# Kernel optimization log

Measured on AMD Instinct MI355X. Metric: run time of the kernel, lower is better.

Reference implementation:

```python
import jax, jax.numpy as jnp
import numpy as np

B, N, D, H = 2, 4096, 512, 8
HD = D // H

def setup_inputs() -> dict:
    key = jax.random.key(0)
    ks = jax.random.split(key, 5)
    s = 1.0 / np.sqrt(D)
    return {
        "x": jax.random.normal(ks[0], (B, N, D), dtype=jnp.float32),
        "W_qkv": jax.random.uniform(ks[1], (D, 3 * D), minval=-s, maxval=s, dtype=jnp.float32),
        "b_qkv": jax.random.uniform(ks[2], (3 * D,), minval=-s, maxval=s, dtype=jnp.float32),
        "W_out": jax.random.uniform(ks[3], (D, D), minval=-s, maxval=s, dtype=jnp.float32),
        "b_out": jax.random.uniform(ks[4], (D,), minval=-s, maxval=s, dtype=jnp.float32),
    }

def reference(x, W_qkv, b_qkv, W_out, b_out):
    Bq, Nq, Dq = x.shape
    scale = HD ** -0.5
    qkv = x @ W_qkv + b_qkv                      # [B,N,3D]
    qkv = qkv.reshape(Bq, Nq, 3, H, HD)
    q, k, v = (jnp.moveaxis(qkv[:, :, i], 2, 1) for i in range(3))  # [B,H,N,hd]
    attn = jnp.einsum('bhqd,bhkd->bhqk', q, k) * scale   # [B,H,N,N]
    causal = jnp.tril(jnp.ones((Nq, Nq), dtype=bool))
    attn = jnp.where(causal, attn, -jnp.inf)
    attn = jax.nn.softmax(attn, axis=-1)
    out = jnp.einsum('bhqk,bhkd->bhqd', attn, v)         # [B,H,N,hd]
    out = jnp.moveaxis(out, 1, 2).reshape(Bq, Nq, Dq)
    return out @ W_out + b_out
```

## Files before the change

kernel.cpp:

```cpp
#include <hip/hip_runtime.h>
#include <hip/hip_bf16.h>


typedef __bf16 bf16_t;
typedef __bf16 bf16x2 __attribute__((ext_vector_type(2)));
typedef __bf16 bf16x4 __attribute__((ext_vector_type(4)));
typedef __bf16 bf16x8 __attribute__((ext_vector_type(8)));
typedef float  f32x4  __attribute__((ext_vector_type(4)));
typedef unsigned int uint32x4 __attribute__((ext_vector_type(4)));

__device__ __forceinline__ void gload_lds16(const bf16_t* g, bf16_t* l) {
    __builtin_amdgcn_global_load_lds(
        (const __attribute__((address_space(1))) void*)g,
        (__attribute__((address_space(3))) void*)l, 16, 0, 0);
}


__device__ __forceinline__ void transpose_tile_body(
    const float* __restrict__ in, bf16_t* __restrict__ out, int N,
    int n0, int k0, int tid, bf16_t (*T)[72])
{
    #pragma unroll
    for (int pass = 0; pass < 4; ++pass) {
        int kk = pass * 16 + (tid >> 4), nn = (tid & 15) * 4;
        float4 v = *(const float4*)(in + (size_t)(k0 + kk) * N + n0 + nn);
        T[nn + 0][kk] = (bf16_t)v.x; T[nn + 1][kk] = (bf16_t)v.y;
        T[nn + 2][kk] = (bf16_t)v.z; T[nn + 3][kk] = (bf16_t)v.w;
    }
    __syncthreads();
    #pragma unroll
    for (int pass = 0; pass < 2; ++pass) {
        int n = pass * 32 + (tid >> 3), c8 = (tid & 7) * 8;
        *(bf16x8*)(out + (size_t)(n0 + n) * 512 + k0 + c8) = *(const bf16x8*)&T[n][c8];
    }
}

__global__ void prep_kernel(const float* __restrict__ x, bf16_t* __restrict__ xb,
                            const float* __restrict__ Wqkv, bf16_t* __restrict__ WqT,
                            const float* __restrict__ Wout, bf16_t* __restrict__ WoT)
{
    __shared__ bf16_t T[64][72];
    const int bid = blockIdx.x, tid = threadIdx.x;
    if (bid < 4096) {
        int i = bid * 256 + tid;
        float4 v = ((const float4*)x)[i];
        bf16x4 o;
        o[0] = (bf16_t)v.x; o[1] = (bf16_t)v.y; o[2] = (bf16_t)v.z; o[3] = (bf16_t)v.w;
        ((bf16x4*)xb)[i] = o;
    } else if (bid < 4288) {
        int idx = bid - 4096;
        transpose_tile_body(Wqkv, WqT, 1536, (idx % 24) * 64, (idx / 24) * 64, tid, T);
    } else {
        int idx = bid - 4288;
        transpose_tile_body(Wout, WoT, 512, (idx & 7) * 64, (idx >> 3) * 64, tid, T);
    }
}


template <int MODE, int TN>
__global__ __launch_bounds__(256) void gemm_bt(
    const bf16_t* __restrict__ A, const bf16_t* __restrict__ Bt,
    const float* __restrict__ bias,
    bf16_t* __restrict__ Qg, bf16_t* __restrict__ Kg, bf16_t* __restrict__ Vtp,
    float* __restrict__ Cout)
{
    constexpr int NI = (TN == 128) ? 4 : 2;
    __shared__ bf16_t smem[128 * 64 + TN * 64];
    bf16_t* As = smem;
    bf16_t* Bs = smem + 128 * 64;
    const int tid  = threadIdx.x;
    const int wid  = tid >> 6, lane = tid & 63, l16 = lane & 15, quad = lane >> 4;
    const int l8   = l16 & 7;
    const int wr   = (TN == 128) ? (wid >> 1) * 64 : wid * 32;
    const int wc   = (TN == 128) ? (wid & 1) * 64 : 0;

    int bx, by;
    {
        const int gx  = gridDim.x;
        const int nwg = gx * gridDim.y;
        const int lin = blockIdx.y * gx + blockIdx.x;
        const int cpx = nwg >> 3;
        const int nl  = (lin & 7) * cpx + (lin >> 3);
        bx = nl % gx; by = nl / gx;
    }
    const int m0   = by * 128, n0 = bx * TN;

    f32x4 acc[NI][4] = {};

    for (int kk = 0; kk < 512; kk += 64) {
        __syncthreads();
        #pragma unroll
        for (int i = 0; i < 4; ++i) {
            int slot = tid + i * 256;
            int row = slot >> 3, cg = (slot & 7) ^ (row & 7);
            gload_lds16(A + (size_t)(m0 + row) * 512 + kk + cg * 8,
                        (bf16_t*)((char*)As + ((i * 256 + (wid << 6)) << 4)));
        }
        #pragma unroll
        for (int i = 0; i < TN / 32; ++i) {
            int slot = tid + i * 256;
            int row = slot >> 3, cg = (slot & 7) ^ (row & 7);
            gload_lds16(Bt + (size_t)(n0 + row) * 512 + kk + cg * 8,
                        (bf16_t*)((char*)Bs + ((i * 256 + (wid << 6)) << 4)));
        }
        __syncthreads();
        #pragma unroll
        for (int s = 0; s < 2; ++s) {
            const int sw = (s * 4 + quad);
            bf16x8 a[NI], b[4];
            #pragma unroll
            for (int i = 0; i < NI; ++i) {
                int row = wr + i * 16 + l16;
                a[i] = *(const bf16x8*)&As[(row * 8 + (sw ^ l8)) * 8];
            }
            #pragma unroll
            for (int j = 0; j < 4; ++j) {
                int row = wc + j * 16 + l16;
                b[j] = *(const bf16x8*)&Bs[(row * 8 + (sw ^ l8)) * 8];
            }
            #pragma unroll
            for (int i = 0; i < NI; ++i)
                #pragma unroll
                for (int j = 0; j < 4; ++j)
                    acc[i][j] = __builtin_amdgcn_mfma_f32_16x16x32_bf16(a[i], b[j], acc[i][j], 0, 0, 0);
        }
    }

    const float qscale = 0.18033688011112042f;

    if (MODE == 0) {
        __syncthreads();
        bf16_t* E = smem;
        const float qs = (n0 < 512) ? qscale : 1.0f;
        #pragma unroll
        for (int i = 0; i < NI; ++i) {
            #pragma unroll
            for (int j = 0; j < 4; ++j) {
                int col = wc + j * 16 + l16;
                float bv = bias[n0 + col];
                #pragma unroll
                for (int r = 0; r < 4; ++r) {
                    int row = wr + i * 16 + quad * 4 + r;
                    int sc = (((col >> 3) ^ (row & 15) ^ ((row >> 3) & 7)) << 3) + (col & 7);
                    E[row * 128 + sc] = (bf16_t)((acc[i][j][r] + bv) * qs);
                }
            }
        }
        __syncthreads();

        const int b_ = m0 >> 12;
        if (n0 < 1024) {
            bf16_t* dst = (n0 < 512) ? Qg : Kg;
            #pragma unroll
            for (int p = 0; p < 8; ++p) {
                int g = p * 256 + tid;
                int c = g & 7, drow = g >> 3;
                int hsel = drow >> 7, nl = drow & 127;
                int col0 = hsel * 64 + c * 8;
                int sc = (((col0 >> 3) ^ (nl & 15) ^ ((nl >> 3) & 7)) << 3);
                bf16x8 v = *(const bf16x8*)&E[nl * 128 + sc];
                int hh = ((n0 + hsel * 64) >> 6) & 7;
                int n = (m0 & 4095) + nl;
                size_t idx = (((size_t)(b_ * 8 + hh) * 4096) + n) * 64 + c * 8;
                *(bf16x8*)(dst + idx) = v;
            }
        } else {
            #pragma unroll
            for (int p = 0; p < 8; ++p) {
                int g = p * 256 + tid;
                int cn8 = g & 15, hdrow = g >> 4;
                int hsel = hdrow >> 6, hd = hdrow & 63;
                int col = hsel * 64 + hd;
                bf16x8 v;
                #pragma unroll
                for (int k = 0; k < 8; ++k) {
                    int row = cn8 * 8 + k;
                    int sc = (((col >> 3) ^ (row & 15) ^ ((row >> 3) & 7)) << 3) + (col & 7);
                    v[k] = E[row * 128 + sc];
                }
                int hh = ((n0 + hsel * 64) >> 6) & 7;
                int nbase = (m0 & 4095) + cn8 * 8;
                size_t idx = ((size_t)(b_ * 8 + hh) * 64 + hd) * 4096 + nbase;
                *(bf16x8*)(Vtp + idx) = v;
            }
        }
    } else {
        #pragma unroll
        for (int i = 0; i < NI; ++i) {
            int mrow = m0 + wr + i * 16 + quad * 4;
            #pragma unroll
            for (int j = 0; j < 4; ++j) {
                int cgl = n0 + wc + j * 16 + l16;
                float bv = bias[cgl];
                #pragma unroll
                for (int r = 0; r < 4; ++r) {
                    int m = mrow + r;
                    Cout[(size_t)m * 512 + cgl] = acc[i][j][r] + bv;
                }
            }
        }
    }
}


__global__ __launch_bounds__(256, 2) void attn_ns2(
    const bf16_t* __restrict__ Qg, const bf16_t* __restrict__ Kg,
    const bf16_t* __restrict__ Vt,
    bf16_t* __restrict__ o_part, float* __restrict__ l_part, int nsplit)
{
    __shared__ bf16_t Ks[2][64][72];
    __shared__ bf16_t Vs[2][64][72];

    const int tid  = threadIdx.x;
    const int w    = tid >> 6, lane = tid & 63, l16 = lane & 15, quad = lane >> 4;
    const int bh   = blockIdx.x & 15, pr = (blockIdx.x >> 4) & 7, h = blockIdx.x >> 7;

    bf16_t* ob = o_part + (size_t)(h * 16 + bh) * 4096 * 64;
    float*  lb = l_part + (size_t)(h * 16 + bh) * 4096;

    const int srow = tid >> 3, scol = (tid & 7) * 8;
    const int srow1 = srow + 32;
    const float MSHIFT = 12.0f;

    bf16x8 ones;
    #pragma unroll
    for (int j = 0; j < 8; ++j) ones[j] = (bf16_t)1.0f;

    uint4 kr0, kr1, vr0, vr1;

#define TILE_PROLOGUE()                                                        \
    const int cur = kt & 1;                                                    \
    *(uint4*)&Ks[cur][srow][scol]  = kr0;                                      \
    *(uint4*)&Ks[cur][srow1][scol] = kr1;                                      \
    *(uint4*)&Vs[cur][srow][scol]  = vr0;                                      \
    *(uint4*)&Vs[cur][srow1][scol] = vr1;                                      \
    __syncthreads();                                                           \
    if (kt + 1 < b1) {                                                         \
        const size_t kb = ((size_t)bh * 4096 + (kt + 1) * 64) * 64;            \
        const size_t vb = (size_t)bh * 64 * 4096 + (kt + 1) * 64;              \
        kr0 = *(const uint4*)(Kg + kb + (size_t)srow * 64 + scol);             \
        kr1 = *(const uint4*)(Kg + kb + (size_t)srow1 * 64 + scol);            \
        vr0 = *(const uint4*)(Vt + vb + (size_t)srow * 4096 + scol);           \
        vr1 = *(const uint4*)(Vt + vb + (size_t)srow1 * 4096 + scol);          \
    }                                                                          \
    bf16x8 kf[4][2], vf[4][2];                                                 \
    _Pragma("unroll")                                                          \
    for (int cb = 0; cb < 4; ++cb) {                                           \
        kf[cb][0] = *(const bf16x8*)&Ks[cur][cb * 16 + l16][quad * 8];         \
        kf[cb][1] = *(const bf16x8*)&Ks[cur][cb * 16 + l16][32 + quad * 8];    \
    }                                                                          \
    _Pragma("unroll")                                                          \
    for (int j = 0; j < 4; ++j) {                                              \
        vf[j][0] = *(const bf16x8*)&Vs[cur][j * 16 + l16][quad * 8];           \
        vf[j][1] = *(const bf16x8*)&Vs[cur][j * 16 + l16][32 + quad * 8];      \
    }

#define SOFTMAX_PERMLANE(sv, pa0, pa1)                                         \
    unsigned int c_[4][2];                                                     \
    _Pragma("unroll")                                                          \
    for (int cb = 0; cb < 4; ++cb) {                                           \
        _Pragma("unroll")                                                      \
        for (int t = 0; t < 2; ++t) {                                          \
            bf16x2 pk2;                                                        \
            pk2[0] = (bf16_t)__builtin_amdgcn_exp2f(sv[cb][2 * t]     - MSHIFT); \
            pk2[1] = (bf16_t)__builtin_amdgcn_exp2f(sv[cb][2 * t + 1] - MSHIFT); \
            c_[cb][t] = __builtin_bit_cast(unsigned int, pk2);                 \
        }                                                                      \
    }                                                                          \
    unsigned int pw0[4], pw1[4];                                               \
    _Pragma("unroll")                                                          \
    for (int t = 0; t < 2; ++t) {                                              \
        auto u  = __builtin_amdgcn_permlane32_swap(c_[0][t], c_[1][t], false, false); \
        auto z  = __builtin_amdgcn_permlane16_swap(u[0], u[1], false, false);  \
        pw0[t] = z[0]; pw0[t + 2] = z[1];                                      \
        auto u2 = __builtin_amdgcn_permlane32_swap(c_[2][t], c_[3][t], false, false); \
        auto z2 = __builtin_amdgcn_permlane16_swap(u2[0], u2[1], false, false); \
        pw1[t] = z2[0]; pw1[t + 2] = z2[1];                                    \
    }                                                                          \
    uint32x4 w0v = {pw0[0], pw0[1], pw0[2], pw0[3]};                           \
    uint32x4 w1v = {pw1[0], pw1[1], pw1[2], pw1[3]};                           \
    bf16x8 pa0 = __builtin_bit_cast(bf16x8, w0v);                              \
    bf16x8 pa1 = __builtin_bit_cast(bf16x8, w1v);

    for (int ph = 0; ph < 2; ++ph) {
        const int st = ph ? (15 - pr) : pr;
        const int T  = 4 * st + 4;
        const int b0 = (h * T) / nsplit, b1 = ((h + 1) * T) / nsplit;
        const int st4 = 4 * st;
        const int fastEnd = (st4 < b1) ? st4 : b1;

        int qrow[4];
        bf16x8 qf[4][2];
        #pragma unroll
        for (int s = 0; s < 4; ++s) {
            qrow[s] = st * 256 + s * 64 + w * 16 + l16;
            const bf16_t* qp = Qg + ((size_t)bh * 4096 + qrow[s]) * 64;
            qf[s][0] = *(const bf16x8*)(qp + quad * 8);
            qf[s][1] = *(const bf16x8*)(qp + 32 + quad * 8);
        }

        f32x4 o[4][4] = {};
        f32x4 lacc[4] = {};

        {
            const size_t kb = ((size_t)bh * 4096 + b0 * 64) * 64;
            const size_t vb = (size_t)bh * 64 * 4096 + b0 * 64;
            kr0 = *(const uint4*)(Kg + kb + (size_t)srow * 64 + scol);
            kr1 = *(const uint4*)(Kg + kb + (size_t)srow1 * 64 + scol);
            vr0 = *(const uint4*)(Vt + vb + (size_t)srow * 4096 + scol);
            vr1 = *(const uint4*)(Vt + vb + (size_t)srow1 * 4096 + scol);
        }
        __syncthreads();

        int kt = b0;

        for (; kt < fastEnd; ++kt) {
            TILE_PROLOGUE();
            #pragma unroll
            for (int s = 0; s < 4; ++s) {
                f32x4 sv[4] = {};
                __builtin_amdgcn_s_setprio(1);
                #pragma unroll
                for (int cb = 0; cb < 4; ++cb) {
                    sv[cb] = __builtin_amdgcn_mfma_f32_16x16x32_bf16(kf[cb][0], qf[s][0], sv[cb], 0, 0, 0);
                    sv[cb] = __builtin_amdgcn_mfma_f32_16x16x32_bf16(kf[cb][1], qf[s][1], sv[cb], 0, 0, 0);
                }
                __builtin_amdgcn_s_setprio(0);
                SOFTMAX_PERMLANE(sv, pa0, pa1);
                __builtin_amdgcn_s_setprio(1);
                #pragma unroll
                for (int j = 0; j < 4; ++j) {
                    o[s][j] = __builtin_amdgcn_mfma_f32_16x16x32_bf16(pa0, vf[j][0], o[s][j], 0, 0, 0);
                    o[s][j] = __builtin_amdgcn_mfma_f32_16x16x32_bf16(pa1, vf[j][1], o[s][j], 0, 0, 0);
                }
                lacc[s] = __builtin_amdgcn_mfma_f32_16x16x32_bf16(pa0, ones, lacc[s], 0, 0, 0);
                lacc[s] = __builtin_amdgcn_mfma_f32_16x16x32_bf16(pa1, ones, lacc[s], 0, 0, 0);
                __builtin_amdgcn_s_setprio(0);
            }
        }

        for (; kt < b1; ++kt) {
            TILE_PROLOGUE();
            #pragma unroll
            for (int s = 0; s < 4; ++s) {
                const int diag = st4 + s;
                if (kt > diag) continue;

                f32x4 sv[4] = {};
                #pragma unroll
                for (int cb = 0; cb < 4; ++cb) {
                    sv[cb] = __builtin_amdgcn_mfma_f32_16x16x32_bf16(kf[cb][0], qf[s][0], sv[cb], 0, 0, 0);
                    sv[cb] = __builtin_amdgcn_mfma_f32_16x16x32_bf16(kf[cb][1], qf[s][1], sv[cb], 0, 0, 0);
                }

                if (kt == diag) {
                    #pragma unroll
                    for (int cb = 0; cb < 4; ++cb) {
                        const int keyg = kt * 64 + cb * 16 + quad * 4;
                        #pragma unroll
                        for (int r = 0; r < 4; ++r)
                            if (keyg + r > qrow[s]) sv[cb][r] = -1e30f;
                    }
                }

                SOFTMAX_PERMLANE(sv, pa0, pa1);
                #pragma unroll
                for (int j = 0; j < 4; ++j) {
                    o[s][j] = __builtin_amdgcn_mfma_f32_16x16x32_bf16(pa0, vf[j][0], o[s][j], 0, 0, 0);
                    o[s][j] = __builtin_amdgcn_mfma_f32_16x16x32_bf16(pa1, vf[j][1], o[s][j], 0, 0, 0);
                }
                lacc[s] = __builtin_amdgcn_mfma_f32_16x16x32_bf16(pa0, ones, lacc[s], 0, 0, 0);
                lacc[s] = __builtin_amdgcn_mfma_f32_16x16x32_bf16(pa1, ones, lacc[s], 0, 0, 0);
            }
        }

        #pragma unroll
        for (int s = 0; s < 4; ++s)
            #pragma unroll
            for (int r = 0; r < 4; ++r) {
                int n = st * 256 + s * 64 + w * 16 + quad * 4 + r;
                #pragma unroll
                for (int j = 0; j < 4; ++j)
                    ob[(size_t)n * 64 + j * 16 + l16] = (bf16_t)o[s][j][r];
                if (l16 == 0) lb[n] = lacc[s][r];
            }
    }
#undef TILE_PROLOGUE
#undef SOFTMAX_PERMLANE
}

__global__ void combine_kernel(const bf16_t* __restrict__ o_part,
                               const float* __restrict__ l_part,
                               bf16_t* __restrict__ Og, int ns)
{
    int t = blockIdx.x * 256 + threadIdx.x;
    int oct = t & 7, n = (t >> 3) & 4095, bh = t >> 15;
    size_t base = ((size_t)bh * 4096 + n) * 64 + oct * 8;
    float s[8] = {};
    float l = 0.f;
    for (int h = 0; h < ns; ++h) {
        bf16x8 v = *(const bf16x8*)(o_part + (size_t)h * 16 * 4096 * 64 + base);
        #pragma unroll
        for (int j = 0; j < 8; ++j) s[j] += (float)v[j];
        l += l_part[(size_t)h * 16 * 4096 + (size_t)bh * 4096 + n];
    }
    float inv = 1.0f / l;
    bf16x8 res;
    #pragma unroll
    for (int j = 0; j < 8; ++j) res[j] = (bf16_t)(s[j] * inv);
    *(bf16x8*)(Og + ((size_t)((bh >> 3) * 4096 + n)) * 512 + (bh & 7) * 64 + oct * 8) = res;
}


extern "C" void kernel_launch(void* const* d_in, const int* in_sizes, int n_in,
                              void* d_out, int out_size, void* d_ws, size_t ws_size,
                              hipStream_t stream) {
    const float* x    = (const float*)d_in[0];
    const float* Wqkv = (const float*)d_in[1];
    const float* bqkv = (const float*)d_in[2];
    const float* Wout = (const float*)d_in[3];
    const float* bout = (const float*)d_in[4];
    float* out = (float*)d_out;

    char* ws = (char*)d_ws;
    bf16_t* xb  = (bf16_t*)(ws);
    bf16_t* WqT = (bf16_t*)(ws + 8388608);
    bf16_t* WoT = (bf16_t*)(ws + 9961472);
    bf16_t* Qg  = (bf16_t*)(ws + 10485760);
    bf16_t* Kg  = (bf16_t*)(ws + 18874368);
    bf16_t* Vt  = (bf16_t*)(ws + 27262976);

    const int nsplit = 4;
    bf16_t* o_part = (bf16_t*)(ws + 35651584);
    float*  l_part = (float*)(ws + 35651584 + (size_t)nsplit * 8388608);

    prep_kernel<<<4352, 256, 0, stream>>>(x, xb, Wqkv, WqT, Wout, WoT);

    gemm_bt<0, 128><<<dim3(12, 64), 256, 0, stream>>>(xb, WqT, bqkv, Qg, Kg, Vt, nullptr);

    attn_ns2<<<128 * nsplit, 256, 0, stream>>>(Qg, Kg, Vt, o_part, l_part, nsplit);
    combine_kernel<<<2048, 256, 0, stream>>>(o_part, l_part, xb , nsplit);

    gemm_bt<1, 64><<<dim3(8, 64), 256, 0, stream>>>(xb, WoT, bout, nullptr, nullptr, nullptr, out);
}
```

Before: 165.2 us.

## Fuse split-KV combine into output projection GEMM A-tile load

Removes the separate combine kernel and does the split reduction inside the output GEMM. Each block first computes 1/l for its rows into shared memory, then sums the partial outputs while staging the A tile into LDS. The GEMM also moves to 128-wide N tiles, so only 256 blocks run and each reads the partial outputs for half as many column blocks. The cost is that async global-to-LDS loads become register loads plus conversion arithmetic, and the low block count may underfill the GPU.

```diff
diff --git a/kernel.cpp b/kernel.cpp
--- a/kernel.cpp
+++ b/kernel.cpp
@@ -62,10 +62,13 @@
     const bf16_t* __restrict__ A, const bf16_t* __restrict__ Bt,
     const float* __restrict__ bias,
     bf16_t* __restrict__ Qg, bf16_t* __restrict__ Kg, bf16_t* __restrict__ Vtp,
-    float* __restrict__ Cout)
+    float* __restrict__ Cout,
+    const bf16_t* __restrict__ OP, const float* __restrict__ LP)
 {
     constexpr int NI = (TN == 128) ? 4 : 2;
+    constexpr int NS = 4;
     __shared__ bf16_t smem[128 * 64 + TN * 64];
+    __shared__ float linv_s[(MODE == 1) ? 1024 : 1];
     bf16_t* As = smem;
     bf16_t* Bs = smem + 128 * 64;
     const int tid  = threadIdx.x;
@@ -84,17 +87,55 @@
         bx = nl % gx; by = nl / gx;
     }
     const int m0   = by * 128, n0 = bx * TN;
+    const int b8   = (m0 >> 12) * 8;
+    const int nbase0 = m0 & 4095;
+
+    if (MODE == 1) {
+        #pragma unroll
+        for (int q = 0; q < 4; ++q) {
+            int idx = tid + q * 256;
+            int hh = idx >> 7, row = idx & 127;
+            const float* lp = LP + (size_t)(b8 + hh) * 4096 + nbase0 + row;
+            float l = 0.f;
+            #pragma unroll
+            for (int sl = 0; sl < NS; ++sl) l += lp[(size_t)sl * 65536];
+            linv_s[idx] = 1.0f / l;
+        }
+    }
 
     f32x4 acc[NI][4] = {};
 
     for (int kk = 0; kk < 512; kk += 64) {
         __syncthreads();
-        #pragma unroll
-        for (int i = 0; i < 4; ++i) {
-            int slot = tid + i * 256;
-            int row = slot >> 3, cg = (slot & 7) ^ (row & 7);
-            gload_lds16(A + (size_t)(m0 + row) * 512 + kk + cg * 8,
-                        (bf16_t*)((char*)As + ((i * 256 + (wid << 6)) << 4)));
+        if (MODE == 1) {
+            const int hh = kk >> 6;
+            const size_t obase = (size_t)(b8 + hh) * 262144;
+            #pragma unroll
+            for (int i = 0; i < 4; ++i) {
+                int slot = tid + i * 256;
+                int row = slot >> 3, cg = (slot & 7) ^ (row & 7);
+                const bf16_t* op = OP + obase + (size_t)(nbase0 + row) * 64 + cg * 8;
+                float s[8] = {};
+                #pragma unroll
+                for (int sl = 0; sl < NS; ++sl) {
+                    bf16x8 v = *(const bf16x8*)(op + (size_t)sl * 4194304);
+                    #pragma unroll
+                    for (int j = 0; j < 8; ++j) s[j] += (float)v[j];
+                }
+                const float inv = linv_s[(hh << 7) + row];
+                bf16x8 o8;
+                #pragma unroll
+                for (int j = 0; j < 8; ++j) o8[j] = (bf16_t)(s[j] * inv);
+                *(bf16x8*)&As[slot * 8] = o8;
+            }
+        } else {
+            #pragma unroll
+            for (int i = 0; i < 4; ++i) {
+                int slot = tid + i * 256;
+                int row = slot >> 3, cg = (slot & 7) ^ (row & 7);
+                gload_lds16(A + (size_t)(m0 + row) * 512 + kk + cg * 8,
+                            (bf16_t*)((char*)As + ((i * 256 + (wid << 6)) << 4)));
+            }
         }
         #pragma unroll
         for (int i = 0; i < TN / 32; ++i) {
@@ -389,28 +430,6 @@
 #undef SOFTMAX_PERMLANE
 }
 
-__global__ void combine_kernel(const bf16_t* __restrict__ o_part,
-                               const float* __restrict__ l_part,
-                               bf16_t* __restrict__ Og, int ns)
-{
-    int t = blockIdx.x * 256 + threadIdx.x;
-    int oct = t & 7, n = (t >> 3) & 4095, bh = t >> 15;
-    size_t base = ((size_t)bh * 4096 + n) * 64 + oct * 8;
-    float s[8] = {};
-    float l = 0.f;
-    for (int h = 0; h < ns; ++h) {
-        bf16x8 v = *(const bf16x8*)(o_part + (size_t)h * 16 * 4096 * 64 + base);
-        #pragma unroll
-        for (int j = 0; j < 8; ++j) s[j] += (float)v[j];
-        l += l_part[(size_t)h * 16 * 4096 + (size_t)bh * 4096 + n];
-    }
-    float inv = 1.0f / l;
-    bf16x8 res;
-    #pragma unroll
-    for (int j = 0; j < 8; ++j) res[j] = (bf16_t)(s[j] * inv);
-    *(bf16x8*)(Og + ((size_t)((bh >> 3) * 4096 + n)) * 512 + (bh & 7) * 64 + oct * 8) = res;
-}
-
 
 extern "C" void kernel_launch(void* const* d_in, const int* in_sizes, int n_in,
                               void* d_out, int out_size, void* d_ws, size_t ws_size,
@@ -436,10 +455,11 @@
 
     prep_kernel<<<4352, 256, 0, stream>>>(x, xb, Wqkv, WqT, Wout, WoT);
 
-    gemm_bt<0, 128><<<dim3(12, 64), 256, 0, stream>>>(xb, WqT, bqkv, Qg, Kg, Vt, nullptr);
+    gemm_bt<0, 128><<<dim3(12, 64), 256, 0, stream>>>(
+        xb, WqT, bqkv, Qg, Kg, Vt, nullptr, nullptr, nullptr);
 
     attn_ns2<<<128 * nsplit, 256, 0, stream>>>(Qg, Kg, Vt, o_part, l_part, nsplit);
-    combine_kernel<<<2048, 256, 0, stream>>>(o_part, l_part, xb , nsplit);
-
-    gemm_bt<1, 64><<<dim3(8, 64), 256, 0, stream>>>(xb, WoT, bout, nullptr, nullptr, nullptr, out);
-}
+
+    gemm_bt<1, 128><<<dim3(4, 64), 256, 0, stream>>>(
+        nullptr, WoT, bout, nullptr, nullptr, nullptr, out, o_part, l_part);
+}
```

Measured after the change: 173.3 us. 1.05x slower.
